# Kernel tuning notes

Hardware: AMD Instinct MI355X
Metric: run time of the kernel (lower is better)

Reference implementation:

```python
import jax, jax.numpy as jnp
import numpy as np

EMB = 768
EPS = 1e-5

def setup_inputs() -> dict:
    key = jax.random.key(0)
    ks = jax.random.split(key, 7)
    B, S, D = 8, 2048, EMB
    s = 1.0 / np.sqrt(D)
    return {
        "h_": jax.random.normal(ks[0], (B, S, D), dtype=jnp.float32),
        "ln_gamma": jnp.ones((D,), jnp.float32),
        "ln_beta": jnp.zeros((D,), jnp.float32),
        "wq": jax.random.normal(ks[1], (D, D), jnp.float32) * s,
        "bq": jax.random.normal(ks[2], (D,), jnp.float32) * 0.01,
        "wk": jax.random.normal(ks[3], (D, D), jnp.float32) * s,
        "bk": jax.random.normal(ks[4], (D,), jnp.float32) * 0.01,
    }

def reference(h_, ln_gamma, ln_beta, wq, bq, wk, bk):
    # LayerNorm over last dim
    mu = jnp.mean(h_, axis=-1, keepdims=True)
    var = jnp.mean(jnp.square(h_ - mu), axis=-1, keepdims=True)
    hn = (h_ - mu) * jax.lax.rsqrt(var + EPS) * ln_gamma + ln_beta
    # Q/K projections (torch Linear: x @ W^T + b; here wq is [D_in, D_out])
    q = jnp.einsum('bsd,de->bse', hn, wq) + bq
    k = jnp.einsum('bsd,de->bse', hn, wk) + bk
    # scores: q @ k^T (no sqrt(d) scaling, matching original)
    w = jnp.einsum('bqd,bkd->bqk', q, k)
    return jax.nn.softmax(w, axis=-1)
```

## Files before the change

### kernel.cpp

```cpp
#include <hip/hip_runtime.h>
#include <stdint.h>

#define EMB   768
#define BATCH 8
#define SEQ   2048
#define ROWS  (BATCH*SEQ)
#define EPS   1e-5f

#define BM 128
#define BN 128
#define BK 32
#define BK2 64

typedef _Float16 half8 __attribute__((ext_vector_type(8)));
typedef _Float16 half4 __attribute__((ext_vector_type(4)));
typedef float    floatx4 __attribute__((ext_vector_type(4)));

__device__ __forceinline__ void g2l16(const void* g, void* l) {
    __builtin_amdgcn_global_load_lds(
        (const __attribute__((address_space(1))) unsigned int*)g,
        (__attribute__((address_space(3))) unsigned int*)l,
        16, 0, 0);
}

__global__ __launch_bounds__(256) void split_w_kernel(
    const float* __restrict__ wq, const float* __restrict__ wk,
    _Float16* __restrict__ wq_hi, _Float16* __restrict__ wq_lo,
    _Float16* __restrict__ wk_hi, _Float16* __restrict__ wk_lo)
{
    const float* src = (blockIdx.y == 0) ? wq : wk;
    _Float16* dh     = (blockIdx.y == 0) ? wq_hi : wk_hi;
    _Float16* dl     = (blockIdx.y == 0) ? wq_lo : wk_lo;
    int i4 = blockIdx.x * 256 + threadIdx.x;
    float4 v = ((const float4*)src)[i4];
    half4 vh, vl;
    float c[4] = {v.x, v.y, v.z, v.w};
#pragma unroll
    for (int t = 0; t < 4; t++) {
        _Float16 hi = (_Float16)c[t];
        vh[t] = hi;
        vl[t] = (_Float16)(c[t] - (float)hi);
    }
    ((half4*)dh)[i4] = vh;
    ((half4*)dl)[i4] = vl;
}

__global__ __launch_bounds__(256) void wtilde_kernel(
    const float* __restrict__ wk, const float* __restrict__ bq,
    float* __restrict__ wt)
{
    int row  = blockIdx.x * 4 + (threadIdx.x >> 6);
    int lane = threadIdx.x & 63;
    const float4* r4 = (const float4*)(wk + (size_t)row * EMB);
    const float4* b4 = (const float4*)bq;
    float s = 0.f;
#pragma unroll
    for (int j = 0; j < 3; j++) {
        float4 a = r4[lane + j * 64];
        float4 b = b4[lane + j * 64];
        s += a.x * b.x + a.y * b.y + a.z * b.z + a.w * b.w;
    }
#pragma unroll
    for (int sh = 1; sh < 64; sh <<= 1) s += __shfl_xor(s, sh, 64);
    if (lane == 0) wt[row] = s;
}

__global__ __launch_bounds__(256) void ln_kernel(
    const float* __restrict__ h,
    const float* __restrict__ gamma,
    const float* __restrict__ beta,
    const float* __restrict__ wt,
    _Float16* __restrict__ hn_hi,
    float* __restrict__ v_out)
{
    int row  = blockIdx.x * 4 + (threadIdx.x >> 6);
    int lane = threadIdx.x & 63;
    const float4* hr4 = (const float4*)(h + (size_t)row * EMB);
    float4 x[3];
    float s1 = 0.f, s2 = 0.f;
#pragma unroll
    for (int j = 0; j < 3; j++) {
        x[j] = hr4[lane + j * 64];
        s1 += x[j].x + x[j].y + x[j].z + x[j].w;
        s2 += x[j].x * x[j].x + x[j].y * x[j].y + x[j].z * x[j].z + x[j].w * x[j].w;
    }
#pragma unroll
    for (int s = 1; s < 64; s <<= 1) {
        s1 += __shfl_xor(s1, s, 64);
        s2 += __shfl_xor(s2, s, 64);
    }
    float mu  = s1 * (1.0f / EMB);
    float var = s2 * (1.0f / EMB) - mu * mu;
    float rs  = rsqrtf(var + EPS);
    _Float16* oh = hn_hi + (size_t)row * EMB;
    float vsum = 0.f;
#pragma unroll
    for (int j = 0; j < 3; j++) {
        int e4 = lane + j * 64;
        float4 g = ((const float4*)gamma)[e4];
        float4 b = ((const float4*)beta)[e4];
        float4 w = ((const float4*)wt)[e4];
        float v[4] = {
            (x[j].x - mu) * rs * g.x + b.x,
            (x[j].y - mu) * rs * g.y + b.y,
            (x[j].z - mu) * rs * g.z + b.z,
            (x[j].w - mu) * rs * g.w + b.w };
        vsum += v[0] * w.x + v[1] * w.y + v[2] * w.z + v[3] * w.w;
        half4 vh;
#pragma unroll
        for (int t = 0; t < 4; t++) vh[t] = (_Float16)v[t];
        *(half4*)(oh + e4 * 4) = vh;
    }
#pragma unroll
    for (int s = 1; s < 64; s <<= 1) vsum += __shfl_xor(vsum, s, 64);
    if (lane == 0) v_out[row] = vsum;
}

__global__ __launch_bounds__(256) void gt_kernel(
    const _Float16* __restrict__ wk_hi, const _Float16* __restrict__ wk_lo,
    const _Float16* __restrict__ wq_hi, const _Float16* __restrict__ wq_lo,
    _Float16* __restrict__ gt_hi, _Float16* __restrict__ gt_lo)
{
    __shared__ __attribute__((aligned(16))) _Float16 Ah_s[BM * BK];
    __shared__ __attribute__((aligned(16))) _Float16 Al_s[BM * BK];
    __shared__ __attribute__((aligned(16))) _Float16 Bh_s[BN * BK];
    __shared__ __attribute__((aligned(16))) _Float16 Bl_s[BN * BK];

    int rowbase = blockIdx.y * BM;
    int colbase = blockIdx.x * BN;
    int tid  = threadIdx.x;
    int lane = tid & 63, wave = tid >> 6;
    int wrow = (wave >> 1) * 64, wcol = (wave & 1) * 64;

    floatx4 acc[4][4];
#pragma unroll
    for (int i = 0; i < 4; i++)
#pragma unroll
        for (int j = 0; j < 4; j++) acc[i][j] = (floatx4){0.f, 0.f, 0.f, 0.f};

    size_t arow = (size_t)(rowbase + tid / 4) * EMB;
    size_t brow = (size_t)(colbase + tid / 4) * EMB;
    int    boff = (((tid % 4) ^ ((tid >> 3) & 3)) * 16);
    const char* gAh = (const char*)(wk_hi + arow) + boff;
    const char* gAl = (const char*)(wk_lo + arow) + boff;
    const char* gBh = (const char*)(wq_hi + brow) + boff;
    const char* gBl = (const char*)(wq_lo + brow) + boff;
    char* lAh = (char*)Ah_s + tid * 16;
    char* lAl = (char*)Al_s + tid * 16;
    char* lBh = (char*)Bh_s + tid * 16;
    char* lBl = (char*)Bl_s + tid * 16;
    const size_t half_stride = (size_t)64 * EMB * 2;

    for (int k0 = 0; k0 < EMB; k0 += BK) {
        __syncthreads();
        g2l16(gAh, lAh); g2l16(gAh + half_stride, lAh + 4096);
        g2l16(gAl, lAl); g2l16(gAl + half_stride, lAl + 4096);
        g2l16(gBh, lBh); g2l16(gBh + half_stride, lBh + 4096);
        g2l16(gBl, lBl); g2l16(gBl + half_stride, lBl + 4096);
        gAh += 64; gAl += 64; gBh += 64; gBl += 64;
        __syncthreads();

        half8 ah[4], al[4], bh[4], bl[4];
#pragma unroll
        for (int i = 0; i < 4; i++) {
            int roff = wrow + i * 16 + (lane & 15);
            int off = roff * 64 + ((((lane >> 4)) ^ ((roff >> 1) & 3)) * 16);
            ah[i] = *(const half8*)((const char*)Ah_s + off);
            al[i] = *(const half8*)((const char*)Al_s + off);
        }
#pragma unroll
        for (int j = 0; j < 4; j++) {
            int coff = wcol + j * 16 + (lane & 15);
            int off = coff * 64 + ((((lane >> 4)) ^ ((coff >> 1) & 3)) * 16);
            bh[j] = *(const half8*)((const char*)Bh_s + off);
            bl[j] = *(const half8*)((const char*)Bl_s + off);
        }
#pragma unroll
        for (int i = 0; i < 4; i++)
#pragma unroll
            for (int j = 0; j < 4; j++) {
                acc[i][j] = __builtin_amdgcn_mfma_f32_16x16x32_f16(ah[i], bh[j], acc[i][j], 0, 0, 0);
                acc[i][j] = __builtin_amdgcn_mfma_f32_16x16x32_f16(ah[i], bl[j], acc[i][j], 0, 0, 0);
                acc[i][j] = __builtin_amdgcn_mfma_f32_16x16x32_f16(al[i], bh[j], acc[i][j], 0, 0, 0);
            }
    }

#pragma unroll
    for (int j = 0; j < 4; j++) {
        int col = colbase + wcol + j * 16 + (lane & 15);
#pragma unroll
        for (int i = 0; i < 4; i++) {
#pragma unroll
            for (int r = 0; r < 4; r++) {
                int row = rowbase + wrow + i * 16 + (lane >> 4) * 4 + r;
                float v = acc[i][j][r];
                _Float16 hi = (_Float16)v;
                gt_hi[(size_t)row * EMB + col] = hi;
                gt_lo[(size_t)row * EMB + col] = (_Float16)(v - (float)hi);
            }
        }
    }
}

__global__ __launch_bounds__(256) void t_kernel(
    const _Float16* __restrict__ hn_hi,
    const _Float16* __restrict__ gt_hi, const _Float16* __restrict__ gt_lo,
    _Float16* __restrict__ t_hi)
{
    __shared__ __attribute__((aligned(16))) _Float16 Ah_s[BM * BK2];
    __shared__ __attribute__((aligned(16))) _Float16 Bh_s[BN * BK2];
    __shared__ __attribute__((aligned(16))) _Float16 Bl_s[BN * BK2];

    int rowbase = blockIdx.y * BM;
    int colbase = blockIdx.x * BN;
    int tid  = threadIdx.x;
    int lane = tid & 63, wave = tid >> 6;
    int wrow = (wave >> 1) * 64, wcol = (wave & 1) * 64;

    floatx4 acc[4][4];
#pragma unroll
    for (int i = 0; i < 4; i++)
#pragma unroll
        for (int j = 0; j < 4; j++) acc[i][j] = (floatx4){0.f, 0.f, 0.f, 0.f};

    size_t arow = (size_t)(rowbase + tid / 8) * EMB;
    size_t brow = (size_t)(colbase + tid / 8) * EMB;
    int    boff = (((tid % 8) ^ ((tid >> 3) & 7)) * 16);
    const char* gAh = (const char*)(hn_hi + arow) + boff;
    const char* gBh = (const char*)(gt_hi + brow) + boff;
    const char* gBl = (const char*)(gt_lo + brow) + boff;
    char* lAh = (char*)Ah_s + tid * 16;
    char* lBh = (char*)Bh_s + tid * 16;
    char* lBl = (char*)Bl_s + tid * 16;
    const size_t pstride = (size_t)32 * EMB * 2;

    for (int k0 = 0; k0 < EMB; k0 += BK2) {
        __syncthreads();
#pragma unroll
        for (int p = 0; p < 4; p++) {
            g2l16(gAh + p * pstride, lAh + p * 4096);
            g2l16(gBh + p * pstride, lBh + p * 4096);
            g2l16(gBl + p * pstride, lBl + p * 4096);
        }
        gAh += 128; gBh += 128; gBl += 128;
        __syncthreads();

#pragma unroll
        for (int ko = 0; ko < 2; ko++) {
            half8 ah[4], bh[4], bl[4];
#pragma unroll
            for (int i = 0; i < 4; i++) {
                int roff = wrow + i * 16 + (lane & 15);
                int off = roff * 128 + ((ko * 64 + (lane >> 4) * 16) ^ ((roff & 7) << 4));
                ah[i] = *(const half8*)((const char*)Ah_s + off);
            }
#pragma unroll
            for (int j = 0; j < 4; j++) {
                int coff = wcol + j * 16 + (lane & 15);
                int off = coff * 128 + ((ko * 64 + (lane >> 4) * 16) ^ ((coff & 7) << 4));
                bh[j] = *(const half8*)((const char*)Bh_s + off);
                bl[j] = *(const half8*)((const char*)Bl_s + off);
            }
#pragma unroll
            for (int i = 0; i < 4; i++)
#pragma unroll
                for (int j = 0; j < 4; j++) {
                    acc[i][j] = __builtin_amdgcn_mfma_f32_16x16x32_f16(ah[i], bh[j], acc[i][j], 0, 0, 0);
                    acc[i][j] = __builtin_amdgcn_mfma_f32_16x16x32_f16(ah[i], bl[j], acc[i][j], 0, 0, 0);
                }
        }
    }

#pragma unroll
    for (int j = 0; j < 4; j++) {
        int col = colbase + wcol + j * 16 + (lane & 15);
#pragma unroll
        for (int i = 0; i < 4; i++) {
#pragma unroll
            for (int r = 0; r < 4; r++) {
                int row = rowbase + wrow + i * 16 + (lane >> 4) * 4 + r;
                t_hi[(size_t)row * EMB + col] = (_Float16)acc[i][j][r];
            }
        }
    }
}

template<bool F16OUT>
__global__ __launch_bounds__(256) void scores_kernel(
    const _Float16* __restrict__ t_hi,
    const _Float16* __restrict__ hn_hi,
    const float* __restrict__ v_in,
    float* __restrict__ out,
    _Float16* __restrict__ pt,
    float2* __restrict__ state)
{
    __shared__ __attribute__((aligned(16))) _Float16 Ah_s[BM * BK2];
    __shared__ __attribute__((aligned(16))) _Float16 Bh_s[BN * BK2];
    __shared__ float red[128][2];

    int b = blockIdx.z;
    size_t base = (size_t)b * SEQ * EMB;
    int rowbase = blockIdx.y * BM;
    int colbase = blockIdx.x * BN;
    int tid  = threadIdx.x;
    int lane = tid & 63, wave = tid >> 6;
    int wrow = (wave >> 1) * 64, wcol = (wave & 1) * 64;

    floatx4 acc[4][4];
#pragma unroll
    for (int i = 0; i < 4; i++)
#pragma unroll
        for (int j = 0; j < 4; j++) acc[i][j] = (floatx4){0.f, 0.f, 0.f, 0.f};

    size_t arow = base + (size_t)(rowbase + tid / 8) * EMB;
    size_t brow = base + (size_t)(colbase + tid / 8) * EMB;
    int    boff = (((tid % 8) ^ ((tid >> 3) & 7)) * 16);
    const char* gAh = (const char*)(t_hi + arow) + boff;
    const char* gBh = (const char*)(hn_hi + brow) + boff;
    char* lAh = (char*)Ah_s + tid * 16;
    char* lBh = (char*)Bh_s + tid * 16;
    const size_t pstride = (size_t)32 * EMB * 2;

    for (int k0 = 0; k0 < EMB; k0 += BK2) {
        __syncthreads();
#pragma unroll
        for (int p = 0; p < 4; p++) {
            g2l16(gAh + p * pstride, lAh + p * 4096);
            g2l16(gBh + p * pstride, lBh + p * 4096);
        }
        gAh += 128; gBh += 128;
        __syncthreads();

#pragma unroll
        for (int ko = 0; ko < 2; ko++) {
            half8 ah[4], bh[4];
#pragma unroll
            for (int i = 0; i < 4; i++) {
                int roff = wrow + i * 16 + (lane & 15);
                int off = roff * 128 + ((ko * 64 + (lane >> 4) * 16) ^ ((roff & 7) << 4));
                ah[i] = *(const half8*)((const char*)Ah_s + off);
            }
#pragma unroll
            for (int j = 0; j < 4; j++) {
                int coff = wcol + j * 16 + (lane & 15);
                int off = coff * 128 + ((ko * 64 + (lane >> 4) * 16) ^ ((coff & 7) << 4));
                bh[j] = *(const half8*)((const char*)Bh_s + off);
            }
#pragma unroll
            for (int i = 0; i < 4; i++)
#pragma unroll
                for (int j = 0; j < 4; j++)
                    acc[i][j] = __builtin_amdgcn_mfma_f32_16x16x32_f16(ah[i], bh[j], acc[i][j], 0, 0, 0);
        }
    }

    const float* vb = v_in + (size_t)b * SEQ + colbase;
#pragma unroll
    for (int j = 0; j < 4; j++) {
        float vv = vb[wcol + j * 16 + (lane & 15)];
#pragma unroll
        for (int i = 0; i < 4; i++)
#pragma unroll
            for (int r = 0; r < 4; r++) acc[i][j][r] += vv;
    }

    float m1[4][4];
#pragma unroll
    for (int i = 0; i < 4; i++)
#pragma unroll
        for (int r = 0; r < 4; r++) {
            float m = fmaxf(fmaxf(acc[i][0][r], acc[i][1][r]), fmaxf(acc[i][2][r], acc[i][3][r]));
#pragma unroll
            for (int s = 1; s < 16; s <<= 1) m = fmaxf(m, __shfl_xor(m, s, 64));
            m1[i][r] = m;
        }
    if ((lane & 15) == 0) {
#pragma unroll
        for (int i = 0; i < 4; i++)
#pragma unroll
            for (int r = 0; r < 4; r++)
                red[wrow + i * 16 + (lane >> 4) * 4 + r][wave & 1] = m1[i][r];
    }
    __syncthreads();
    float mrow[4][4];
#pragma unroll
    for (int i = 0; i < 4; i++)
#pragma unroll
        for (int r = 0; r < 4; r++) {
            int rr = wrow + i * 16 + (lane >> 4) * 4 + r;
            mrow[i][r] = fmaxf(red[rr][0], red[rr][1]);
        }
    __syncthreads();

    float ls[4][4];
#pragma unroll
    for (int i = 0; i < 4; i++)
#pragma unroll
        for (int r = 0; r < 4; r++) {
            float s = 0.f;
#pragma unroll
            for (int j = 0; j < 4; j++) {
                float e = __expf(acc[i][j][r] - mrow[i][r]);
                acc[i][j][r] = e;
                s += e;
            }
#pragma unroll
            for (int sh = 1; sh < 16; sh <<= 1) s += __shfl_xor(s, sh, 64);
            ls[i][r] = s;
        }
    if ((lane & 15) == 0) {
#pragma unroll
        for (int i = 0; i < 4; i++)
#pragma unroll
            for (int r = 0; r < 4; r++)
                red[wrow + i * 16 + (lane >> 4) * 4 + r][wave & 1] = ls[i][r];
    }
    __syncthreads();

    size_t outbase = (size_t)b * SEQ * SEQ;
#pragma unroll
    for (int i = 0; i < 4; i++)
#pragma unroll
        for (int j = 0; j < 4; j++)
#pragma unroll
            for (int r = 0; r < 4; r++) {
                int row = rowbase + wrow + i * 16 + (lane >> 4) * 4 + r;
                int col = colbase + wcol + j * 16 + (lane & 15);
                if (F16OUT)
                    pt[outbase + (size_t)row * SEQ + col] = (_Float16)acc[i][j][r];
                else
                    out[outbase + (size_t)row * SEQ + col] = acc[i][j][r];
            }

    if ((wave & 1) == 0 && (lane & 15) == 0) {
#pragma unroll
        for (int i = 0; i < 4; i++)
#pragma unroll
            for (int r = 0; r < 4; r++) {
                int rr = wrow + i * 16 + (lane >> 4) * 4 + r;
                float l = red[rr][0] + red[rr][1];
                state[((size_t)b * SEQ + rowbase + rr) * 16 + blockIdx.x] =
                    make_float2(mrow[i][r], l);
            }
    }
}

template<bool F16IN>
__global__ __launch_bounds__(256) void fixup_kernel(
    float* __restrict__ out,
    const _Float16* __restrict__ pt,
    const float2* __restrict__ state)
{
    int row  = blockIdx.x * 4 + (threadIdx.x >> 6);
    int lane = threadIdx.x & 63;
    float2 v = state[(size_t)row * 16 + (lane & 15)];
    float M = v.x;
#pragma unroll
    for (int s = 1; s < 16; s <<= 1) M = fmaxf(M, __shfl_xor(M, s, 64));
    float e  = __expf(v.x - M);
    float Lp = v.y * e;
#pragma unroll
    for (int s = 1; s < 16; s <<= 1) Lp += __shfl_xor(Lp, s, 64);
    float fv = e / Lp;

    if (F16IN) {
        const half8* p8 = (const half8*)(pt + (size_t)row * SEQ);
        float4* o4 = (float4*)(out + (size_t)row * SEQ);
#pragma unroll
        for (int c0 = 0; c0 < 4; c0++) {
            int i8 = c0 * 64 + lane;
            float s = __shfl(fv, i8 >> 4, 64);
            half8 h = p8[i8];
            float4 a, bqv;
            a.x = (float)h[0] * s; a.y = (float)h[1] * s;
            a.z = (float)h[2] * s; a.w = (float)h[3] * s;
            bqv.x = (float)h[4] * s; bqv.y = (float)h[5] * s;
            bqv.z = (float)h[6] * s; bqv.w = (float)h[7] * s;
            o4[i8 * 2]     = a;
            o4[i8 * 2 + 1] = bqv;
        }
    } else {
        float4* o4 = (float4*)(out + (size_t)row * SEQ);
#pragma unroll
        for (int c0 = 0; c0 < 8; c0++) {
            int i4 = c0 * 64 + lane;
            float s = __shfl(fv, i4 >> 5, 64);
            float4 w = o4[i4];
            w.x *= s; w.y *= s; w.z *= s; w.w *= s;
            o4[i4] = w;
        }
    }
}

extern "C" void kernel_launch(void* const* d_in, const int* in_sizes, int n_in,
                              void* d_out, int out_size, void* d_ws, size_t ws_size,
                              hipStream_t stream)
{
    const float* h  = (const float*)d_in[0];
    const float* g  = (const float*)d_in[1];
    const float* be = (const float*)d_in[2];
    const float* wq = (const float*)d_in[3];
    const float* bq = (const float*)d_in[4];
    const float* wk = (const float*)d_in[5];
    const float* bk = (const float*)d_in[6];
    (void)bk;
    float* out = (float*)d_out;

    char* ws = (char*)d_ws;
    const size_t SZ  = (size_t)ROWS * EMB * 2;
    const size_t WSZ = (size_t)EMB * EMB * 2;
    _Float16* hn_hi = (_Float16*)(ws);
    _Float16* t_hi  = (_Float16*)(ws + SZ);
    char* wbase = ws + 2 * SZ;
    _Float16* wq_hi = (_Float16*)(wbase);
    _Float16* wq_lo = (_Float16*)(wbase + WSZ);
    _Float16* wk_hi = (_Float16*)(wbase + 2 * WSZ);
    _Float16* wk_lo = (_Float16*)(wbase + 3 * WSZ);
    _Float16* gt_hi = (_Float16*)(wbase + 4 * WSZ);
    _Float16* gt_lo = (_Float16*)(wbase + 5 * WSZ);
    char* sbase = wbase + 6 * WSZ;
    float*  wt = (float*)(sbase);
    float*  v  = (float*)(sbase + 4096);
    float2* st = (float2*)(sbase + 4096 + 65536);
    char*   ptb = sbase + 4096 + 65536 + (size_t)ROWS * 16 * sizeof(float2);
    const size_t PTSZ = (size_t)BATCH * SEQ * SEQ * 2;
    _Float16* pt = (_Float16*)ptb;
    bool use_f16 = ws_size >= (size_t)(ptb - ws) + PTSZ;

    split_w_kernel<<<dim3(576, 2), 256, 0, stream>>>(wq, wk, wq_hi, wq_lo, wk_hi, wk_lo);
    wtilde_kernel<<<dim3(EMB / 4), 256, 0, stream>>>(wk, bq, wt);
    ln_kernel<<<dim3(ROWS / 4), 256, 0, stream>>>(h, g, be, wt, hn_hi, v);
    gt_kernel<<<dim3(EMB / BN, EMB / BM), 256, 0, stream>>>(wk_hi, wk_lo, wq_hi, wq_lo, gt_hi, gt_lo);
    t_kernel<<<dim3(EMB / BN, ROWS / BM), 256, 0, stream>>>(hn_hi, gt_hi, gt_lo, t_hi);
    if (use_f16) {
        scores_kernel<true><<<dim3(SEQ / BN, SEQ / BM, BATCH), 256, 0, stream>>>(t_hi, hn_hi, v, out, pt, st);
        fixup_kernel<true><<<dim3(ROWS / 4), 256, 0, stream>>>(out, pt, st);
    } else {
        scores_kernel<false><<<dim3(SEQ / BN, SEQ / BM, BATCH), 256, 0, stream>>>(t_hi, hn_hi, v, out, nullptr, st);
        fixup_kernel<false><<<dim3(ROWS / 4), 256, 0, stream>>>(out, nullptr, st);
    }
}
```

Before: 373.5 us.

## Double-buffer LDS tiles in t_kernel and scores_kernel to overlap loads with MFMA

Both GEMM kernels now keep two LDS stages. The next K-tile is prefetched with global_load_lds while the current tile feeds MFMA, and explicit vmcnt waits plus s_barrier replace the paired __syncthreads. t_kernel also drops its K-step from 64 to 32 and changes its swizzle so three double-buffered operands fit in LDS. The aim is to hide global load latency behind compute, at the cost of more LDS per block, which may reduce occupancy in scores_kernel, and of hand-tuned waitcnt counts that must match the number of issued loads.

Result: no change. 369.7 us (-1.0%).

```diff
diff --git a/kernel.cpp b/kernel.cpp
--- a/kernel.cpp
+++ b/kernel.cpp
@@ -207,9 +207,9 @@
     const _Float16* __restrict__ gt_hi, const _Float16* __restrict__ gt_lo,
     _Float16* __restrict__ t_hi)
 {
-    __shared__ __attribute__((aligned(16))) _Float16 Ah_s[BM * BK2];
-    __shared__ __attribute__((aligned(16))) _Float16 Bh_s[BN * BK2];
-    __shared__ __attribute__((aligned(16))) _Float16 Bl_s[BN * BK2];
+    __shared__ __attribute__((aligned(16))) _Float16 Ah_s[2][BM * BK];
+    __shared__ __attribute__((aligned(16))) _Float16 Bh_s[2][BN * BK];
+    __shared__ __attribute__((aligned(16))) _Float16 Bl_s[2][BN * BK];
 
     int rowbase = blockIdx.y * BM;
     int colbase = blockIdx.x * BN;
@@ -223,52 +223,62 @@
 #pragma unroll
         for (int j = 0; j < 4; j++) acc[i][j] = (floatx4){0.f, 0.f, 0.f, 0.f};
 
-    size_t arow = (size_t)(rowbase + tid / 8) * EMB;
-    size_t brow = (size_t)(colbase + tid / 8) * EMB;
-    int    boff = (((tid % 8) ^ ((tid >> 3) & 7)) * 16);
+    size_t arow = (size_t)(rowbase + tid / 4) * EMB;
+    size_t brow = (size_t)(colbase + tid / 4) * EMB;
+    int    boff = (((tid % 4) ^ ((tid >> 3) & 3)) * 16);
     const char* gAh = (const char*)(hn_hi + arow) + boff;
     const char* gBh = (const char*)(gt_hi + brow) + boff;
     const char* gBl = (const char*)(gt_lo + brow) + boff;
-    char* lAh = (char*)Ah_s + tid * 16;
-    char* lBh = (char*)Bh_s + tid * 16;
-    char* lBl = (char*)Bl_s + tid * 16;
-    const size_t pstride = (size_t)32 * EMB * 2;
-
-    for (int k0 = 0; k0 < EMB; k0 += BK2) {
-        __syncthreads();
-#pragma unroll
-        for (int p = 0; p < 4; p++) {
-            g2l16(gAh + p * pstride, lAh + p * 4096);
-            g2l16(gBh + p * pstride, lBh + p * 4096);
-            g2l16(gBl + p * pstride, lBl + p * 4096);
-        }
-        gAh += 128; gBh += 128; gBl += 128;
-        __syncthreads();
-
-#pragma unroll
-        for (int ko = 0; ko < 2; ko++) {
-            half8 ah[4], bh[4], bl[4];
-#pragma unroll
-            for (int i = 0; i < 4; i++) {
-                int roff = wrow + i * 16 + (lane & 15);
-                int off = roff * 128 + ((ko * 64 + (lane >> 4) * 16) ^ ((roff & 7) << 4));
-                ah[i] = *(const half8*)((const char*)Ah_s + off);
-            }
+    const size_t half_stride = (size_t)64 * EMB * 2;
+
+    auto STAGE = [&](int c) {
+        char* lA = (char*)Ah_s[c] + tid * 16;
+        char* lB = (char*)Bh_s[c] + tid * 16;
+        char* lC = (char*)Bl_s[c] + tid * 16;
+        g2l16(gAh, lA); g2l16(gAh + half_stride, lA + 4096);
+        g2l16(gBh, lB); g2l16(gBh + half_stride, lB + 4096);
+        g2l16(gBl, lC); g2l16(gBl + half_stride, lC + 4096);
+        gAh += 64; gBh += 64; gBl += 64;
+    };
+
+    const int NT = EMB / BK;
+    STAGE(0);
+#pragma unroll 2
+    for (int t = 0; t < NT; t++) {
+        int cur = t & 1;
+        asm volatile("" ::: "memory");
+        if (t < NT - 1) {
+            STAGE(cur ^ 1);
+            asm volatile("s_waitcnt vmcnt(6)" ::: "memory");
+        } else {
+            asm volatile("s_waitcnt vmcnt(0)" ::: "memory");
+        }
+        __builtin_amdgcn_s_barrier();
+        asm volatile("" ::: "memory");
+
+        half8 ah[4], bh[4], bl[4];
+#pragma unroll
+        for (int i = 0; i < 4; i++) {
+            int roff = wrow + i * 16 + (lane & 15);
+            int off = roff * 64 + ((((lane >> 4)) ^ ((roff >> 1) & 3)) * 16);
+            ah[i] = *(const half8*)((const char*)Ah_s[cur] + off);
+        }
+#pragma unroll
+        for (int j = 0; j < 4; j++) {
+            int coff = wcol + j * 16 + (lane & 15);
+            int off = coff * 64 + ((((lane >> 4)) ^ ((coff >> 1) & 3)) * 16);
+            bh[j] = *(const half8*)((const char*)Bh_s[cur] + off);
+            bl[j] = *(const half8*)((const char*)Bl_s[cur] + off);
+        }
+#pragma unroll
+        for (int i = 0; i < 4; i++)
 #pragma unroll
             for (int j = 0; j < 4; j++) {
-                int coff = wcol + j * 16 + (lane & 15);
-                int off = coff * 128 + ((ko * 64 + (lane >> 4) * 16) ^ ((coff & 7) << 4));
-                bh[j] = *(const half8*)((const char*)Bh_s + off);
-                bl[j] = *(const half8*)((const char*)Bl_s + off);
-            }
-#pragma unroll
-            for (int i = 0; i < 4; i++)
-#pragma unroll
-                for (int j = 0; j < 4; j++) {
-                    acc[i][j] = __builtin_amdgcn_mfma_f32_16x16x32_f16(ah[i], bh[j], acc[i][j], 0, 0, 0);
-                    acc[i][j] = __builtin_amdgcn_mfma_f32_16x16x32_f16(ah[i], bl[j], acc[i][j], 0, 0, 0);
-                }
-        }
+                acc[i][j] = __builtin_amdgcn_mfma_f32_16x16x32_f16(ah[i], bh[j], acc[i][j], 0, 0, 0);
+                acc[i][j] = __builtin_amdgcn_mfma_f32_16x16x32_f16(ah[i], bl[j], acc[i][j], 0, 0, 0);
+            }
+        asm volatile("" ::: "memory");
+        __builtin_amdgcn_s_barrier();
     }
 
 #pragma unroll
@@ -294,8 +304,8 @@
     _Float16* __restrict__ pt,
     float2* __restrict__ state)
 {
-    __shared__ __attribute__((aligned(16))) _Float16 Ah_s[BM * BK2];
-    __shared__ __attribute__((aligned(16))) _Float16 Bh_s[BN * BK2];
+    __shared__ __attribute__((aligned(16))) _Float16 Ah_s[2][BM * BK2];
+    __shared__ __attribute__((aligned(16))) _Float16 Bh_s[2][BN * BK2];
     __shared__ float red[128][2];
 
     int b = blockIdx.z;
@@ -317,19 +327,33 @@
     int    boff = (((tid % 8) ^ ((tid >> 3) & 7)) * 16);
     const char* gAh = (const char*)(t_hi + arow) + boff;
     const char* gBh = (const char*)(hn_hi + brow) + boff;
-    char* lAh = (char*)Ah_s + tid * 16;
-    char* lBh = (char*)Bh_s + tid * 16;
     const size_t pstride = (size_t)32 * EMB * 2;
 
-    for (int k0 = 0; k0 < EMB; k0 += BK2) {
-        __syncthreads();
+    auto STAGE = [&](int c) {
+        char* lA = (char*)Ah_s[c] + tid * 16;
+        char* lB = (char*)Bh_s[c] + tid * 16;
 #pragma unroll
         for (int p = 0; p < 4; p++) {
-            g2l16(gAh + p * pstride, lAh + p * 4096);
-            g2l16(gBh + p * pstride, lBh + p * 4096);
+            g2l16(gAh + p * pstride, lA + p * 4096);
+            g2l16(gBh + p * pstride, lB + p * 4096);
         }
         gAh += 128; gBh += 128;
-        __syncthreads();
+    };
+
+    const int NT = EMB / BK2;
+    STAGE(0);
+#pragma unroll 2
+    for (int t = 0; t < NT; t++) {
+        int cur = t & 1;
+        asm volatile("" ::: "memory");
+        if (t < NT - 1) {
+            STAGE(cur ^ 1);
+            asm volatile("s_waitcnt vmcnt(8)" ::: "memory");
+        } else {
+            asm volatile("s_waitcnt vmcnt(0)" ::: "memory");
+        }
+        __builtin_amdgcn_s_barrier();
+        asm volatile("" ::: "memory");
 
 #pragma unroll
         for (int ko = 0; ko < 2; ko++) {
@@ -338,13 +362,13 @@
             for (int i = 0; i < 4; i++) {
                 int roff = wrow + i * 16 + (lane & 15);
                 int off = roff * 128 + ((ko * 64 + (lane >> 4) * 16) ^ ((roff & 7) << 4));
-                ah[i] = *(const half8*)((const char*)Ah_s + off);
+                ah[i] = *(const half8*)((const char*)Ah_s[cur] + off);
             }
 #pragma unroll
             for (int j = 0; j < 4; j++) {
                 int coff = wcol + j * 16 + (lane & 15);
                 int off = coff * 128 + ((ko * 64 + (lane >> 4) * 16) ^ ((coff & 7) << 4));
-                bh[j] = *(const half8*)((const char*)Bh_s + off);
+                bh[j] = *(const half8*)((const char*)Bh_s[cur] + off);
             }
 #pragma unroll
             for (int i = 0; i < 4; i++)
@@ -352,6 +376,8 @@
                 for (int j = 0; j < 4; j++)
                     acc[i][j] = __builtin_amdgcn_mfma_f32_16x16x32_f16(ah[i], bh[j], acc[i][j], 0, 0, 0);
         }
+        asm volatile("" ::: "memory");
+        __builtin_amdgcn_s_barrier();
     }
 
     const float* vb = v_in + (size_t)b * SEQ + colbase;
```

## Double-buffer scores GEMM LDS tiles with async prefetch and BK=32

Applied to the files above, without the earlier changes.

Replaces the single-buffered BK=64 K loop in the scores kernel with a two-stage LDS double buffer at BK=32. The next tile is issued via global_load_lds before waiting on the current one with an explicit vmcnt, so global loads can overlap the MFMA work. The LDS swizzle is adapted to 64-byte rows. The trade-off is twice as many loop iterations and barriers, and correctness now depends on hand-written waitcnt counts.

Measured after the change: 381.2 us. +2.0%, slower.

```diff
diff --git a/kernel.cpp b/kernel.cpp
--- a/kernel.cpp
+++ b/kernel.cpp
@@ -294,8 +294,8 @@
     _Float16* __restrict__ pt,
     float2* __restrict__ state)
 {
-    __shared__ __attribute__((aligned(16))) _Float16 Ah_s[BM * BK2];
-    __shared__ __attribute__((aligned(16))) _Float16 Bh_s[BN * BK2];
+    __shared__ __attribute__((aligned(16))) _Float16 Ah_s[2][BM * BK];
+    __shared__ __attribute__((aligned(16))) _Float16 Bh_s[2][BN * BK];
     __shared__ float red[128][2];
 
     int b = blockIdx.z;
@@ -312,46 +312,56 @@
 #pragma unroll
         for (int j = 0; j < 4; j++) acc[i][j] = (floatx4){0.f, 0.f, 0.f, 0.f};
 
-    size_t arow = base + (size_t)(rowbase + tid / 8) * EMB;
-    size_t brow = base + (size_t)(colbase + tid / 8) * EMB;
-    int    boff = (((tid % 8) ^ ((tid >> 3) & 7)) * 16);
+    size_t arow = base + (size_t)(rowbase + tid / 4) * EMB;
+    size_t brow = base + (size_t)(colbase + tid / 4) * EMB;
+    int    boff = (((tid % 4) ^ ((tid >> 3) & 3)) * 16);
     const char* gAh = (const char*)(t_hi + arow) + boff;
     const char* gBh = (const char*)(hn_hi + brow) + boff;
-    char* lAh = (char*)Ah_s + tid * 16;
-    char* lBh = (char*)Bh_s + tid * 16;
-    const size_t pstride = (size_t)32 * EMB * 2;
-
-    for (int k0 = 0; k0 < EMB; k0 += BK2) {
-        __syncthreads();
-#pragma unroll
-        for (int p = 0; p < 4; p++) {
-            g2l16(gAh + p * pstride, lAh + p * 4096);
-            g2l16(gBh + p * pstride, lBh + p * 4096);
-        }
-        gAh += 128; gBh += 128;
-        __syncthreads();
-
-#pragma unroll
-        for (int ko = 0; ko < 2; ko++) {
-            half8 ah[4], bh[4];
-#pragma unroll
-            for (int i = 0; i < 4; i++) {
-                int roff = wrow + i * 16 + (lane & 15);
-                int off = roff * 128 + ((ko * 64 + (lane >> 4) * 16) ^ ((roff & 7) << 4));
-                ah[i] = *(const half8*)((const char*)Ah_s + off);
-            }
-#pragma unroll
-            for (int j = 0; j < 4; j++) {
-                int coff = wcol + j * 16 + (lane & 15);
-                int off = coff * 128 + ((ko * 64 + (lane >> 4) * 16) ^ ((coff & 7) << 4));
-                bh[j] = *(const half8*)((const char*)Bh_s + off);
-            }
-#pragma unroll
-            for (int i = 0; i < 4; i++)
-#pragma unroll
-                for (int j = 0; j < 4; j++)
-                    acc[i][j] = __builtin_amdgcn_mfma_f32_16x16x32_f16(ah[i], bh[j], acc[i][j], 0, 0, 0);
-        }
+    const size_t half_stride = (size_t)64 * EMB * 2;
+
+    auto STAGE = [&](int c) {
+        char* lA = (char*)Ah_s[c] + tid * 16;
+        char* lB = (char*)Bh_s[c] + tid * 16;
+        g2l16(gAh, lA); g2l16(gAh + half_stride, lA + 4096);
+        g2l16(gBh, lB); g2l16(gBh + half_stride, lB + 4096);
+        gAh += 64; gBh += 64;
+    };
+
+    const int NT = EMB / BK;
+    STAGE(0);
+#pragma unroll 2
+    for (int t = 0; t < NT; t++) {
+        int cur = t & 1;
+        asm volatile("" ::: "memory");
+        if (t < NT - 1) {
+            STAGE(cur ^ 1);
+            asm volatile("s_waitcnt vmcnt(4)" ::: "memory");
+        } else {
+            asm volatile("s_waitcnt vmcnt(0)" ::: "memory");
+        }
+        __builtin_amdgcn_s_barrier();
+        asm volatile("" ::: "memory");
+
+        half8 ah[4], bh[4];
+#pragma unroll
+        for (int i = 0; i < 4; i++) {
+            int roff = wrow + i * 16 + (lane & 15);
+            int off = roff * 64 + ((((lane >> 4)) ^ ((roff >> 1) & 3)) * 16);
+            ah[i] = *(const half8*)((const char*)Ah_s[cur] + off);
+        }
+#pragma unroll
+        for (int j = 0; j < 4; j++) {
+            int coff = wcol + j * 16 + (lane & 15);
+            int off = coff * 64 + ((((lane >> 4)) ^ ((coff >> 1) & 3)) * 16);
+            bh[j] = *(const half8*)((const char*)Bh_s[cur] + off);
+        }
+#pragma unroll
+        for (int i = 0; i < 4; i++)
+#pragma unroll
+            for (int j = 0; j < 4; j++)
+                acc[i][j] = __builtin_amdgcn_mfma_f32_16x16x32_f16(ah[i], bh[j], acc[i][j], 0, 0, 0);
+        asm volatile("" ::: "memory");
+        __builtin_amdgcn_s_barrier();
     }
 
     const float* vb = v_in + (size_t)b * SEQ + colbase;
```
